# Optimization experiments

Hardware: AMD Instinct MI355X
Metric: run time of the kernel (lower is better)

Reference implementation:

```python
import jax, jax.numpy as jnp
import numpy as np

DIM = 1024
NUM_HEADS = 16
HEAD_DIM = DIM // NUM_HEADS
B, T = 2, 2048


def setup_inputs() -> dict:
    key = jax.random.key(0)
    ks = jax.random.split(key, 7)
    x = jax.random.normal(ks[0], (B, T, DIM), dtype=jnp.float32)
    # causal mask, broadcastable over batch and heads
    mask = jnp.tril(jnp.ones((T, T), dtype=bool))[None, None, :, :]
    # rope tables for half rotary angles, tiled to head_dim (cat of two halves)
    pos = jnp.arange(T, dtype=jnp.float32)[:, None]
    inv_freq = 1.0 / (10000.0 ** (jnp.arange(0, HEAD_DIM, 2, dtype=jnp.float32) / HEAD_DIM))
    ang = pos * inv_freq[None, :]                      # [T, hd/2]
    ang = jnp.concatenate([ang, ang], axis=-1)         # [T, hd]
    rope_sin = jnp.sin(ang)[None, None, :, :]
    rope_cos = jnp.cos(ang)[None, None, :, :]
    s = 0.02
    qkv_w = jax.random.normal(ks[1], (DIM, 3 * DIM), dtype=jnp.float32) * s
    qkv_b = jnp.zeros((3 * DIM,), dtype=jnp.float32)
    proj_w = jax.random.normal(ks[2], (DIM, DIM), dtype=jnp.float32) * s
    proj_b = jnp.zeros((DIM,), dtype=jnp.float32)
    return {"x": x, "mask": mask, "rope_sin": rope_sin, "rope_cos": rope_cos,
            "qkv_w": qkv_w, "qkv_b": qkv_b, "proj_w": proj_w, "proj_b": proj_b}


def _rotate_half(t):
    half = t.shape[-1] // 2
    return jnp.concatenate([-t[..., half:], t[..., :half]], axis=-1)


def _apply_rope(t, sin, cos):
    return t * cos + _rotate_half(t) * sin


def reference(x, mask, rope_sin, rope_cos, qkv_w, qkv_b, proj_w, proj_b):
    Bb, Tt, C = x.shape
    qkv = x @ qkv_w + qkv_b                            # [B, T, 3C]
    q, k, v = jnp.split(qkv, 3, axis=-1)
    def split_heads(t):                                # [B, T, C] -> [B, H, T, hd]
        return t.reshape(Bb, Tt, NUM_HEADS, HEAD_DIM).transpose(0, 2, 1, 3)
    q, k, v = split_heads(q), split_heads(k), split_heads(v)
    sin = rope_sin[:, :, :Tt, :]
    cos = rope_cos[:, :, :Tt, :]
    q = _apply_rope(q, sin, cos)
    k = _apply_rope(k, sin, cos)
    att = jnp.einsum("bhqd,bhkd->bhqk", q, k) / (HEAD_DIM ** 0.5)
    att = jnp.where(mask, att, -jnp.inf)
    att = jax.nn.softmax(att, axis=-1)
    y = jnp.einsum("bhqk,bhkd->bhqd", att, v)          # [B, H, T, hd]
    y = y.transpose(0, 2, 1, 3).reshape(Bb, Tt, C)
    return y @ proj_w + proj_b
```

## Files before the change

### kernel.cpp

```cpp
#include <hip/hip_runtime.h>

typedef unsigned short u16;
typedef u16 u16x8 __attribute__((ext_vector_type(8)));
typedef __bf16 bf16x8 __attribute__((ext_vector_type(8)));
typedef float f32x4 __attribute__((ext_vector_type(4)));

#define T_SEQ 2048
#define DIM 1024
#define NH 16
#define HD 64

#define MFMA(a, b, c) __builtin_amdgcn_mfma_f32_16x16x32_bf16(a, b, c, 0, 0, 0)

__device__ __forceinline__ u16 f2bf(float f) {
  unsigned u = __builtin_bit_cast(unsigned, f);
  u = u + 0x7fffu + ((u >> 16) & 1u);
  return (u16)(u >> 16);
}

__device__ __forceinline__ bf16x8 ld8(const u16* p) {
  return __builtin_bit_cast(bf16x8, *(const u16x8*)p);
}

__device__ __forceinline__ void gload_lds16(const u16* g, u16* l) {
  __builtin_amdgcn_global_load_lds((const __attribute__((address_space(1))) void*)(g),
                                   (__attribute__((address_space(3))) void*)(l),
                                   16, 0, 0);
}

__global__ void k_prep(const float* __restrict__ X, u16* __restrict__ Y,
                       const float* __restrict__ Wq, u16* __restrict__ WqT,
                       const float* __restrict__ Wp, u16* __restrict__ WpT) {
  __shared__ float tile[32][33];
  int bid = blockIdx.x;
  if (bid < 4096) {
    int i = (bid * 256 + threadIdx.x) * 4;
    float4 f = *(const float4*)&X[i];
    ushort4 o = make_ushort4(f2bf(f.x), f2bf(f.y), f2bf(f.z), f2bf(f.w));
    *(ushort4*)&Y[i] = o;
    return;
  }
  const float* W; u16* WT; int K = 1024, N, bx, by;
  if (bid < 4096 + 3072) { int t = bid - 4096; W = Wq; WT = WqT; N = 3072; bx = t % 96; by = t / 96; }
  else                   { int t = bid - 7168; W = Wp; WT = WpT; N = 1024; bx = t % 32; by = t / 32; }
  int tx = threadIdx.x & 31, ty = threadIdx.x >> 5;
  int c0 = bx * 32, r0 = by * 32;
#pragma unroll
  for (int r = 0; r < 4; r++)
    tile[ty + r * 8][tx] = W[(r0 + ty + r * 8) * N + c0 + tx];
  __syncthreads();
#pragma unroll
  for (int r = 0; r < 4; r++)
    WT[(c0 + ty + r * 8) * K + r0 + tx] = f2bf(tile[tx][ty + r * 8]);
}


#define GEMM_STAGE(buf, kk)                                                       \
  {                                                                               \
    _Pragma("unroll") for (int p = 0; p < 2; p++) {                               \
      int rr = w * 32 + p * 16;                                                   \
      gload_lds16(&Agp[(size_t)(rowBase + rr + srow) * Kd + (kk) + schunk],       \
                  &As[buf][rr * 32]);                                             \
      gload_lds16(&Bgp[(size_t)(colBase + rr + srow) * Kd + (kk) + schunk],       \
                  &Bs[buf][rr * 32]);                                             \
    }                                                                             \
  }

#define GEMM_COMPUTE(buf)                                                         \
  {                                                                               \
    bf16x8 af[4], bfv[4];                                                         \
    _Pragma("unroll") for (int i = 0; i < 4; i++) {                               \
      af[i] = ld8(&As[buf][(wm * 64 + i * 16 + l15) * 32 + quad * 8]);            \
      bfv[i] = ld8(&Bs[buf][(wn * 64 + i * 16 + l15) * 32 + quad * 8]);           \
    }                                                                             \
    _Pragma("unroll") for (int i = 0; i < 4; i++)                                 \
        _Pragma("unroll") for (int j = 0; j < 4; j++)                             \
            acc[i][j] = MFMA(af[i], bfv[j], acc[i][j]);                           \
  }

#define GEMM_CORE(Aptr, BTptr, Kdim, bxv, byv)                                    \
  const int tid = threadIdx.x;                                                    \
  const int lane = tid & 63, w = tid >> 6;                                        \
  const int l15 = lane & 15, quad = lane >> 4;                                    \
  const int wm = w >> 1, wn = w & 1;                                              \
  const int rowBase = (byv) * 128;                                                \
  const int colBase = (bxv) * 128;                                                \
  const u16* Agp = (Aptr);                                                        \
  const u16* Bgp = (BTptr);                                                       \
  const int Kd = (Kdim);                                                          \
  f32x4 acc[4][4];                                                                \
  _Pragma("unroll") for (int i = 0; i < 4; i++)                                   \
      _Pragma("unroll") for (int j = 0; j < 4; j++)                               \
          acc[i][j] = (f32x4){0.f, 0.f, 0.f, 0.f};                                \
  const int srow = lane >> 2;                 \
  const int schunk = (lane & 3) * 8;    \
  GEMM_STAGE(0, 0)                                                                \
  __syncthreads();                                    \
  for (int k0 = 0; k0 < Kd; k0 += 64) {                                          \
    if (k0 + 32 < Kd) GEMM_STAGE(1, k0 + 32)              \
    GEMM_COMPUTE(0)                                       \
    __syncthreads();             \
    if (k0 + 64 < Kd) GEMM_STAGE(0, k0 + 64)              \
    GEMM_COMPUTE(1)                                       \
    __syncthreads();                                                             \
  }

#define EPLD 136

__global__ __launch_bounds__(256) void k_gemm_qkv(
    const u16* __restrict__ A, const u16* __restrict__ BT,
    const float* __restrict__ bias,
    const float* __restrict__ rsin, const float* __restrict__ rcos,
    u16* __restrict__ qb, u16* __restrict__ kb, u16* __restrict__ vtb) {
  __shared__ __align__(16) u16 LDSBUF[128 * EPLD];
  u16 (*As)[128 * 32] = (u16(*)[128 * 32])(LDSBUF);
  u16 (*Bs)[128 * 32] = (u16(*)[128 * 32])(LDSBUF + 8192);
  const int n = blockIdx.x, xcd = n & 7, s = n >> 3;
  const int cg = xcd & 1, rg = xcd >> 1;
  const int bxv = cg * 12 + (s >> 3);
  const int byv = rg * 8 + (s & 7);
  GEMM_CORE(A, BT, DIM, bxv, byv)

#pragma unroll
  for (int j = 0; j < 4; j++) {
    float bv = bias[colBase + wn * 64 + j * 16 + l15];
#pragma unroll
    for (int i = 0; i < 4; i++)
#pragma unroll
      for (int r = 0; r < 4; r++) acc[i][j][r] += bv;
  }

  const int colW = colBase + wn * 64;
  const int sec = colW >> 10;

  if (sec == 2) {
#pragma unroll
    for (int i = 0; i < 4; i++)
#pragma unroll
      for (int r = 0; r < 4; r++) {
        int tl = wm * 64 + i * 16 + quad * 4 + r;
#pragma unroll
        for (int j = 0; j < 4; j++) {
          int d2 = wn * 64 + j * 16 + l15;
          LDSBUF[d2 * EPLD + tl] = f2bf(acc[i][j][r]);
        }
      }
  } else {
#pragma unroll
    for (int i = 0; i < 4; i++)
#pragma unroll
      for (int r = 0; r < 4; r++) {
        int tl = wm * 64 + i * 16 + quad * 4 + r;
        int t = (rowBase + tl) & 2047;
#pragma unroll
        for (int j = 0; j < 4; j++) {
          int d = j * 16 + l15;
          float v = acc[i][j][r];
          float pr = acc[i][j ^ 2][r];
          float rot = (j < 2) ? -pr : pr;
          float rv = v * rcos[t * HD + d] + rot * rsin[t * HD + d];
          if (sec == 0) rv *= 0.125f;
          LDSBUF[tl * EPLD + wn * 64 + d] = f2bf(rv);
        }
      }
  }
  __syncthreads();

  const int hb = (colBase & 1023) >> 6;
  const int b = rowBase >> 11, t0 = rowBase & 2047;
  if (sec == 2) {
#pragma unroll
    for (int p = 0; p < 8; p++) {
      int drow = (tid >> 4) + p * 16;
      int tc = (tid & 15) * 8;
      int hh = hb + (drow >> 6), d = drow & 63;
      u16x8 v = *(const u16x8*)&LDSBUF[drow * EPLD + tc];
      *(u16x8*)&vtb[((size_t)(b * NH + hh) * HD + d) * T_SEQ + t0 + tc] = v;
    }
  } else {
    u16* dst = (sec == 0) ? qb : kb;
#pragma unroll
    for (int p = 0; p < 8; p++) {
      int row = (tid >> 4) + p * 16;
      int dc = (tid & 15) * 8;
      int hh = hb + (dc >> 6), d = dc & 63;
      u16x8 v = *(const u16x8*)&LDSBUF[row * EPLD + dc];
      *(u16x8*)&dst[((size_t)(b * NH + hh) * T_SEQ + t0 + row) * HD + d] = v;
    }
  }
}

__global__ __launch_bounds__(256) void k_gemm_proj(
    const u16* __restrict__ A, const u16* __restrict__ BT,
    const float* __restrict__ bias, float* __restrict__ C) {
  __shared__ __align__(16) u16 LDSBUF[16384];
  u16 (*As)[128 * 32] = (u16(*)[128 * 32])(LDSBUF);
  u16 (*Bs)[128 * 32] = (u16(*)[128 * 32])(LDSBUF + 8192);
  const int n = blockIdx.x, xcd = n & 7, s = n >> 3;
  const int cg = xcd & 1, rg = xcd >> 1;
  const int bxv = cg * 4 + (s >> 3);
  const int byv = rg * 8 + (s & 7);
  GEMM_CORE(A, BT, DIM, bxv, byv)

#pragma unroll
  for (int i = 0; i < 4; i++)
#pragma unroll
    for (int r = 0; r < 4; r++) {
      int grow = rowBase + wm * 64 + i * 16 + quad * 4 + r;
#pragma unroll
      for (int j = 0; j < 4; j++) {
        int col = colBase + wn * 64 + j * 16 + l15;
        C[grow * DIM + col] = acc[i][j][r] + bias[col];
      }
    }
}

#define KLD 72
#define VLD 136

__global__ __launch_bounds__(256) void k_attn(
    const u16* __restrict__ qb, const u16* __restrict__ kb,
    const u16* __restrict__ vtb, u16* __restrict__ yb) {
  __shared__ __align__(16) u16 Qs[64 * KLD];
  __shared__ __align__(16) u16 Ks[128 * KLD];
  __shared__ __align__(16) u16 VTs[64 * VLD];
  __shared__ __align__(16) u16 Ps[4][16 * VLD];
  const int tid = threadIdx.x;
  const int lane = tid & 63, w = tid >> 6;
  const int l15 = lane & 15, quad = lane >> 4;
  const int bh = blockIdx.x;
  const int qt = 31 - blockIdx.y;

  const u16* qp = qb + (size_t)bh * T_SEQ * HD;
  const u16* kp = kb + (size_t)bh * T_SEQ * HD;
  const u16* vp = vtb + (size_t)bh * HD * T_SEQ;

  {
    int sr = tid >> 3, sc = (tid & 7) * 8;
#pragma unroll
    for (int p = 0; p < 2; p++) {
      int r = sr + p * 32;
      *(u16x8*)&Qs[r * KLD + sc] = *(const u16x8*)&qp[(qt * 64 + r) * HD + sc];
    }
  }
  __syncthreads();
  bf16x8 qa0 = ld8(&Qs[(w * 16 + l15) * KLD + quad * 8]);
  bf16x8 qa1 = ld8(&Qs[(w * 16 + l15) * KLD + 32 + quad * 8]);

  f32x4 o[4];
#pragma unroll
  for (int j = 0; j < 4; j++) o[j] = (f32x4){0.f, 0.f, 0.f, 0.f};
  float li[4] = {0.f, 0.f, 0.f, 0.f};

  const int nch = (qt + 2) >> 1;
  const int qrow_base = qt * 64 + w * 16 + quad * 4;

  for (int c = 0; c < nch; c++) {
    {
      int sr = tid >> 3, sc = (tid & 7) * 8;
#pragma unroll
      for (int p = 0; p < 4; p++) {
        int r = sr + p * 32;
        *(u16x8*)&Ks[r * KLD + sc] = *(const u16x8*)&kp[(c * 128 + r) * HD + sc];
      }
      int vr = tid >> 4, vc = (tid & 15) * 8;
#pragma unroll
      for (int p = 0; p < 4; p++) {
        int r = vr + p * 16;
        *(u16x8*)&VTs[r * VLD + vc] = *(const u16x8*)&vp[r * T_SEQ + c * 128 + vc];
      }
    }
    __syncthreads();

    f32x4 s[8];
#pragma unroll
    for (int j = 0; j < 8; j++) {
      s[j] = (f32x4){0.f, 0.f, 0.f, 0.f};
      bf16x8 b0 = ld8(&Ks[(j * 16 + l15) * KLD + quad * 8]);
      bf16x8 b1 = ld8(&Ks[(j * 16 + l15) * KLD + 32 + quad * 8]);
      s[j] = MFMA(qa0, b0, s[j]);
      s[j] = MFMA(qa1, b1, s[j]);
    }

    u16* ps = &Ps[w][0];
    const bool lastc = (c == nch - 1);
#pragma unroll
    for (int r = 0; r < 4; r++) {
#pragma unroll
      for (int j = 0; j < 8; j++) {
        float e = __expf(s[j][r]);
        if (lastc && (c * 128 + j * 16 + l15 > qrow_base + r)) e = 0.f;
        li[r] += e;
        ps[(quad * 4 + r) * VLD + j * 16 + l15] = f2bf(e);
      }
    }

#pragma unroll
    for (int c4 = 0; c4 < 4; c4++) {
      bf16x8 pa = ld8(&ps[l15 * VLD + c4 * 32 + quad * 8]);
#pragma unroll
      for (int j2 = 0; j2 < 4; j2++) {
        bf16x8 vb = ld8(&VTs[(j2 * 16 + l15) * VLD + c4 * 32 + quad * 8]);
        o[j2] = MFMA(pa, vb, o[j2]);
      }
    }
    __syncthreads();
  }

#pragma unroll
  for (int r = 0; r < 4; r++) {
#pragma unroll
    for (int off = 8; off >= 1; off >>= 1) li[r] += __shfl_xor(li[r], off, 16);
    li[r] = 1.0f / li[r];
  }

#pragma unroll
  for (int j = 0; j < 4; j++)
#pragma unroll
    for (int r = 0; r < 4; r++)
      Qs[(w * 16 + quad * 4 + r) * KLD + j * 16 + l15] = f2bf(o[j][r] * li[r]);
  __syncthreads();

  const int b = bh >> 4, h = bh & 15;
  {
    int sr = tid >> 3, sc = (tid & 7) * 8;
#pragma unroll
    for (int p = 0; p < 2; p++) {
      int row = sr + p * 32;
      int t = qt * 64 + row;
      *(u16x8*)&yb[((size_t)(b * T_SEQ + t) * NH + h) * HD + sc] =
          *(const u16x8*)&Qs[row * KLD + sc];
    }
  }
}

extern "C" void kernel_launch(void* const* d_in, const int* in_sizes, int n_in,
                              void* d_out, int out_size, void* d_ws, size_t ws_size,
                              hipStream_t stream) {
  const float* x      = (const float*)d_in[0];
  const float* rsin   = (const float*)d_in[2];
  const float* rcos   = (const float*)d_in[3];
  const float* qkv_w  = (const float*)d_in[4];
  const float* qkv_b  = (const float*)d_in[5];
  const float* proj_w = (const float*)d_in[6];
  const float* proj_b = (const float*)d_in[7];
  float* out = (float*)d_out;

  char* ws = (char*)d_ws;
  u16* x_bf  = (u16*)(ws);
  u16* qkvT  = (u16*)(ws + (8ull << 20));
  u16* projT = (u16*)(ws + (14ull << 20));
  u16* q_buf = (u16*)(ws + (16ull << 20));
  u16* k_buf = (u16*)(ws + (24ull << 20));
  u16* vT    = (u16*)(ws + (32ull << 20));
  u16* y_buf = (u16*)(ws + (40ull << 20));

  hipLaunchKernelGGL(k_prep, dim3(8192), dim3(256), 0, stream,
                     x, x_bf, qkv_w, qkvT, proj_w, projT);
  hipLaunchKernelGGL(k_gemm_qkv, dim3(768), dim3(256), 0, stream,
                     x_bf, qkvT, qkv_b, rsin, rcos, q_buf, k_buf, vT);
  hipLaunchKernelGGL(k_attn, dim3(32, 32), dim3(256), 0, stream,
                     q_buf, k_buf, vT, y_buf);
  hipLaunchKernelGGL(k_gemm_proj, dim3(256), dim3(256), 0, stream,
                     y_buf, projT, proj_b, out);
}
```

Measured before the change: 209.6 us.

## Prefetch K/V into registers, swizzle P rows, reuse LDS for Q and output

The attention kernel now loads the next K/V chunk from global memory into registers while computing on the current chunk, then writes it to LDS after the PV step. This overlaps global memory latency with MFMA work. The Q staging and output staging buffers are folded into the P buffer, which cuts LDS use, and the kernel adds launch_bounds occupancy 3. P rows are written with a row swizzle to reduce LDS bank conflicts, and f2bf now uses the native bf16 conversion. The costs are higher register pressure from the prefetch registers and an extra barrier per chunk.

```diff
diff --git a/kernel.cpp b/kernel.cpp
--- a/kernel.cpp
+++ b/kernel.cpp
@@ -13,9 +13,7 @@
 #define MFMA(a, b, c) __builtin_amdgcn_mfma_f32_16x16x32_bf16(a, b, c, 0, 0, 0)
 
 __device__ __forceinline__ u16 f2bf(float f) {
-  unsigned u = __builtin_bit_cast(unsigned, f);
-  u = u + 0x7fffu + ((u >> 16) & 1u);
-  return (u16)(u >> 16);
+  return __builtin_bit_cast(u16, static_cast<__bf16>(f));
 }
 
 __device__ __forceinline__ bf16x8 ld8(const u16* p) {
@@ -53,7 +51,6 @@
   for (int r = 0; r < 4; r++)
     WT[(c0 + ty + r * 8) * K + r0 + tx] = f2bf(tile[tx][ty + r * 8]);
 }
-
 
 #define GEMM_STAGE(buf, kk)                                                       \
   {                                                                               \
@@ -218,13 +215,12 @@
 #define KLD 72
 #define VLD 136
 
-__global__ __launch_bounds__(256) void k_attn(
+__global__ __launch_bounds__(256, 3) void k_attn(
     const u16* __restrict__ qb, const u16* __restrict__ kb,
     const u16* __restrict__ vtb, u16* __restrict__ yb) {
-  __shared__ __align__(16) u16 Qs[64 * KLD];
   __shared__ __align__(16) u16 Ks[128 * KLD];
   __shared__ __align__(16) u16 VTs[64 * VLD];
-  __shared__ __align__(16) u16 Ps[4][16 * VLD];
+  __shared__ __align__(16) u16 Ps[64 * VLD];
   const int tid = threadIdx.x;
   const int lane = tid & 63, w = tid >> 6;
   const int l15 = lane & 15, quad = lane >> 4;
@@ -235,42 +231,53 @@
   const u16* kp = kb + (size_t)bh * T_SEQ * HD;
   const u16* vp = vtb + (size_t)bh * HD * T_SEQ;
 
+  const int nch = (qt + 2) >> 1;
+  const int qrow_base = qt * 64 + w * 16 + quad * 4;
+
+  const int sr = tid >> 3, sc = (tid & 7) * 8;
+  const int vr = tid >> 4, vc = (tid & 15) * 8;
+
+  u16x8 kreg[4], vreg[4];
+#define LOADKV(c)                                                              \
+  {                                                                            \
+    _Pragma("unroll") for (int p = 0; p < 4; p++)                              \
+        kreg[p] = *(const u16x8*)&kp[((c) * 128 + sr + p * 32) * HD + sc];     \
+    _Pragma("unroll") for (int p = 0; p < 4; p++)                              \
+        vreg[p] = *(const u16x8*)&vp[(vr + p * 16) * T_SEQ + (c) * 128 + vc];  \
+  }
+#define WRITEKV()                                                              \
+  {                                                                            \
+    _Pragma("unroll") for (int p = 0; p < 4; p++)                              \
+        *(u16x8*)&Ks[(sr + p * 32) * KLD + sc] = kreg[p];                      \
+    _Pragma("unroll") for (int p = 0; p < 4; p++)                              \
+        *(u16x8*)&VTs[(vr + p * 16) * VLD + vc] = vreg[p];                     \
+  }
+
+  LOADKV(0)
+
   {
-    int sr = tid >> 3, sc = (tid & 7) * 8;
 #pragma unroll
     for (int p = 0; p < 2; p++) {
       int r = sr + p * 32;
-      *(u16x8*)&Qs[r * KLD + sc] = *(const u16x8*)&qp[(qt * 64 + r) * HD + sc];
-    }
-  }
-  __syncthreads();
-  bf16x8 qa0 = ld8(&Qs[(w * 16 + l15) * KLD + quad * 8]);
-  bf16x8 qa1 = ld8(&Qs[(w * 16 + l15) * KLD + 32 + quad * 8]);
+      *(u16x8*)&Ps[r * KLD + sc] = *(const u16x8*)&qp[(qt * 64 + r) * HD + sc];
+    }
+  }
+  __syncthreads();
+  bf16x8 qa0 = ld8(&Ps[(w * 16 + l15) * KLD + quad * 8]);
+  bf16x8 qa1 = ld8(&Ps[(w * 16 + l15) * KLD + 32 + quad * 8]);
+  WRITEKV()
+  __syncthreads();
 
   f32x4 o[4];
 #pragma unroll
   for (int j = 0; j < 4; j++) o[j] = (f32x4){0.f, 0.f, 0.f, 0.f};
   float li[4] = {0.f, 0.f, 0.f, 0.f};
 
-  const int nch = (qt + 2) >> 1;
-  const int qrow_base = qt * 64 + w * 16 + quad * 4;
+  u16* ps = &Ps[w * 16 * VLD];
+  const int srd = ((l15 & 1) << 3) | ((l15 >> 2) << 1) | ((l15 >> 1) & 1);
 
   for (int c = 0; c < nch; c++) {
-    {
-      int sr = tid >> 3, sc = (tid & 7) * 8;
-#pragma unroll
-      for (int p = 0; p < 4; p++) {
-        int r = sr + p * 32;
-        *(u16x8*)&Ks[r * KLD + sc] = *(const u16x8*)&kp[(c * 128 + r) * HD + sc];
-      }
-      int vr = tid >> 4, vc = (tid & 15) * 8;
-#pragma unroll
-      for (int p = 0; p < 4; p++) {
-        int r = vr + p * 16;
-        *(u16x8*)&VTs[r * VLD + vc] = *(const u16x8*)&vp[r * T_SEQ + c * 128 + vc];
-      }
-    }
-    __syncthreads();
+    if (c + 1 < nch) LOADKV(c + 1)
 
     f32x4 s[8];
 #pragma unroll
@@ -282,22 +289,22 @@
       s[j] = MFMA(qa1, b1, s[j]);
     }
 
-    u16* ps = &Ps[w][0];
     const bool lastc = (c == nch - 1);
 #pragma unroll
     for (int r = 0; r < 4; r++) {
+      const int swr = ((r & 1) << 3) | (quad << 1) | (r >> 1);
 #pragma unroll
       for (int j = 0; j < 8; j++) {
         float e = __expf(s[j][r]);
         if (lastc && (c * 128 + j * 16 + l15 > qrow_base + r)) e = 0.f;
         li[r] += e;
-        ps[(quad * 4 + r) * VLD + j * 16 + l15] = f2bf(e);
+        ps[swr * VLD + j * 16 + l15] = f2bf(e);
       }
     }
 
 #pragma unroll
     for (int c4 = 0; c4 < 4; c4++) {
-      bf16x8 pa = ld8(&ps[l15 * VLD + c4 * 32 + quad * 8]);
+      bf16x8 pa = ld8(&ps[srd * VLD + c4 * 32 + quad * 8]);
 #pragma unroll
       for (int j2 = 0; j2 < 4; j2++) {
         bf16x8 vb = ld8(&VTs[(j2 * 16 + l15) * VLD + c4 * 32 + quad * 8]);
@@ -305,6 +312,10 @@
       }
     }
     __syncthreads();
+    if (c + 1 < nch) {
+      WRITEKV()
+      __syncthreads();
+    }
   }
 
 #pragma unroll
@@ -317,19 +328,23 @@
 #pragma unroll
   for (int j = 0; j < 4; j++)
 #pragma unroll
-    for (int r = 0; r < 4; r++)
-      Qs[(w * 16 + quad * 4 + r) * KLD + j * 16 + l15] = f2bf(o[j][r] * li[r]);
+    for (int r = 0; r < 4; r++) {
+      const int swr = ((r & 1) << 3) | (quad << 1) | (r >> 1);
+      ps[swr * VLD + j * 16 + l15] = f2bf(o[j][r] * li[r]);
+    }
   __syncthreads();
 
   const int b = bh >> 4, h = bh & 15;
   {
-    int sr = tid >> 3, sc = (tid & 7) * 8;
+    int sr2 = tid >> 3, sc2 = (tid & 7) * 8;
 #pragma unroll
     for (int p = 0; p < 2; p++) {
-      int row = sr + p * 32;
+      int row = sr2 + p * 32;
+      int m = row & 15;
+      int srow = ((m & 1) << 3) | ((m >> 2) << 1) | ((m >> 1) & 1);
       int t = qt * 64 + row;
-      *(u16x8*)&yb[((size_t)(b * T_SEQ + t) * NH + h) * HD + sc] =
-          *(const u16x8*)&Qs[row * KLD + sc];
+      *(u16x8*)&yb[((size_t)(b * T_SEQ + t) * NH + h) * HD + sc2] =
+          *(const u16x8*)&Ps[((row & 48) | srow) * VLD + sc2];
     }
   }
 }
```

After: 201.7 us. 3.8% less time.
